# Kernel tuning notes

Measured on AMD Instinct MI355X. Metric: run time of the kernel, lower is better.

## Reference

```python
import math
import jax, jax.numpy as jnp
import numpy as np

B, S, D, H = 64, 577, 768, 12
DH = D // H          # 64 per-head dim
FF = 4 * D           # 3072 intermediate
EPS = 1e-6


def layernorm(x, g, b):
    mu = jnp.mean(x, axis=-1, keepdims=True)
    var = jnp.mean(jnp.square(x - mu), axis=-1, keepdims=True)
    return (x - mu) * jax.lax.rsqrt(var + EPS) * g + b


def gelu_tanh(x):
    # NewGELUActivation: 0.5*x*(1+tanh(sqrt(2/pi)*(x+0.044715*x^3)))
    c = math.sqrt(2.0 / math.pi)
    return 0.5 * x * (1.0 + jnp.tanh(c * (x + 0.044715 * x ** 3)))


def setup_inputs() -> dict:
    key = jax.random.key(0)
    ks = jax.random.split(key, 16)
    s_d = 1.0 / math.sqrt(D)
    s_ff = 1.0 / math.sqrt(FF)
    return {
        "x": jax.random.normal(ks[0], (B, S, D), jnp.float32),
        "ln1_g": jnp.ones((D,), jnp.float32),
        "ln1_b": jnp.zeros((D,), jnp.float32),
        # per-head Q/K/V weights stacked: [H, D, DH] (equivalent to H separate Linears)
        "Wq": jax.random.normal(ks[1], (H, D, DH), jnp.float32) * s_d,
        "bq": jax.random.normal(ks[2], (H, DH), jnp.float32) * 0.01,
        "Wk": jax.random.normal(ks[3], (H, D, DH), jnp.float32) * s_d,
        "bk": jax.random.normal(ks[4], (H, DH), jnp.float32) * 0.01,
        "Wv": jax.random.normal(ks[5], (H, D, DH), jnp.float32) * s_d,
        "bv": jax.random.normal(ks[6], (H, DH), jnp.float32) * 0.01,
        "Wo": jax.random.normal(ks[7], (D, D), jnp.float32) * s_d,
        "bo": jax.random.normal(ks[8], (D,), jnp.float32) * 0.01,
        "ln2_g": jnp.ones((D,), jnp.float32),
        "ln2_b": jnp.zeros((D,), jnp.float32),
        "W1": jax.random.normal(ks[9], (D, FF), jnp.float32) * s_d,
        "b1": jax.random.normal(ks[10], (FF,), jnp.float32) * 0.01,
        "W2": jax.random.normal(ks[11], (FF, D), jnp.float32) * s_ff,
        "b2": jax.random.normal(ks[12], (D,), jnp.float32) * 0.01,
    }


def reference(x, ln1_g, ln1_b, Wq, bq, Wk, bk, Wv, bv, Wo, bo,
              ln2_g, ln2_b, W1, b1, W2, b2):
    # --- pre-norm MHA ---
    h = layernorm(x, ln1_g, ln1_b)                       # [B,S,D]
    q = jnp.einsum('bsd,hde->bhse', h, Wq) + bq[:, None, :]
    k = jnp.einsum('bsd,hde->bhse', h, Wk) + bk[:, None, :]
    v = jnp.einsum('bsd,hde->bhse', h, Wv) + bv[:, None, :]
    scores = jnp.einsum('bhse,bhte->bhst', q, k) / math.sqrt(DH)
    probs = jax.nn.softmax(scores, axis=-1)              # [B,H,S,S]
    attn = jnp.einsum('bhst,bhte->bhse', probs, v)       # [B,H,S,DH]
    # concat heads in head order -> [B,S,H*DH]
    concat = attn.transpose(0, 2, 1, 3).reshape(B, S, H * DH)
    x = x + concat @ Wo + bo
    # --- pre-norm MLP ---
    m = layernorm(x, ln2_g, ln2_b)
    m = gelu_tanh(m @ W1 + b1) @ W2 + b2
    return x + m
```

## Files before the change

kernel.cpp:

```cpp
#include <hip/hip_runtime.h>
#include <stdint.h>

constexpr int BZ   = 64;
constexpr int SEQ  = 577;
constexpr int DM   = 768;
constexpr int NH   = 12;
constexpr int HD   = 64;
constexpr int FFD  = 3072;
constexpr int ROWS = BZ * SEQ;
constexpr int BHN  = BZ * NH;
constexpr int VTS  = 640;

typedef __attribute__((ext_vector_type(8))) short bf16x8;
typedef __attribute__((ext_vector_type(4))) float f32x4;

static __device__ __forceinline__ unsigned short f2bf(float f) {
  union { float f; uint32_t u; } v; v.f = f;
  uint32_t r = (v.u + 0x7FFFu + ((v.u >> 16) & 1u)) >> 16;
  return (unsigned short)r;
}

static __device__ __forceinline__ f32x4 mfma16(bf16x8 a, bf16x8 b, f32x4 c) {
  return __builtin_amdgcn_mfma_f32_16x16x32_bf16(a, b, c, 0, 0, 0);
}

static __device__ __forceinline__ void gload_lds16(const unsigned short* g, unsigned short* l) {
  __builtin_amdgcn_global_load_lds((const __attribute__((address_space(1))) unsigned int*)g,
                                   (__attribute__((address_space(3))) unsigned int*)l, 16, 0, 0);
}

__global__ __launch_bounds__(256) void prep_qkv(const float* __restrict__ Wq,
                                                const float* __restrict__ Wk,
                                                const float* __restrict__ Wv,
                                                unsigned short* __restrict__ dst) {
  int tid = blockIdx.x * 256 + threadIdx.x;
  int n = tid / DM, k = tid - n * DM;
  int seg = n / DM;
  int within = n - seg * DM;
  int h = within >> 6, e = within & 63;
  const float* W = (seg == 0) ? Wq : (seg == 1) ? Wk : Wv;
  dst[tid] = f2bf(W[((size_t)h * DM + k) * HD + e]);
}

__global__ __launch_bounds__(256) void prep_t(const float* __restrict__ src,
                                              unsigned short* __restrict__ dst,
                                              int N, int K) {
  int tid = blockIdx.x * 256 + threadIdx.x;
  if (tid >= N * K) return;
  int n = tid / K, k = tid - n * K;
  dst[tid] = f2bf(src[(size_t)k * N + n]);
}

__global__ __launch_bounds__(256) void ln_bf16(const float* __restrict__ X,
                                               const float* __restrict__ g,
                                               const float* __restrict__ b,
                                               unsigned short* __restrict__ out) {
  int row  = blockIdx.x * 4 + (threadIdx.x >> 6);
  int lane = threadIdx.x & 63;
  const float* x = X + (size_t)row * DM;
  float4 v[3];
  float s = 0.f, s2 = 0.f;
#pragma unroll
  for (int i = 0; i < 3; i++) {
    v[i] = *(const float4*)(x + i * 256 + lane * 4);
    s  += v[i].x + v[i].y + v[i].z + v[i].w;
    s2 += v[i].x * v[i].x + v[i].y * v[i].y + v[i].z * v[i].z + v[i].w * v[i].w;
  }
#pragma unroll
  for (int o = 1; o < 64; o <<= 1) { s += __shfl_xor(s, o); s2 += __shfl_xor(s2, o); }
  float mu  = s * (1.f / DM);
  float var = s2 * (1.f / DM) - mu * mu;
  float inv = rsqrtf(var + 1e-6f);
#pragma unroll
  for (int i = 0; i < 3; i++) {
    int c = i * 256 + lane * 4;
    float4 gg = *(const float4*)(g + c);
    float4 bb = *(const float4*)(b + c);
    ushort4 o4;
    o4.x = f2bf((v[i].x - mu) * inv * gg.x + bb.x);
    o4.y = f2bf((v[i].y - mu) * inv * gg.y + bb.y);
    o4.z = f2bf((v[i].z - mu) * inv * gg.z + bb.z);
    o4.w = f2bf((v[i].w - mu) * inv * gg.w + bb.w);
    *(ushort4*)(out + (size_t)row * DM + c) = o4;
  }
}

template <int EPI>
__global__ __launch_bounds__(512, 2) void gemm_bt(
    const unsigned short* __restrict__ A, const unsigned short* __restrict__ Bt,
    int M, int N, int K, int nbn,
    const float* __restrict__ bias0, const float* __restrict__ bias1,
    const float* __restrict__ bias2, const float* __restrict__ xres,
    float* __restrict__ outf,
    unsigned short* __restrict__ ob0, unsigned short* __restrict__ ob1,
    unsigned short* __restrict__ ob2) {
  __shared__ __align__(16) unsigned short sA[4][256 * 32];
  __shared__ __align__(16) unsigned short sB[4][256 * 32];
  const int tid  = threadIdx.x;
  const int wave = tid >> 6;
  const int lane = tid & 63;
  const int l15 = lane & 15, quad = lane >> 4;
  const int wmi = wave >> 2;
  const int wni = wave & 3;

  const int nb = gridDim.x;
  const int L = blockIdx.x;
  const int per = nb >> 3, rem = nb & 7;
  const int x8 = L & 7, i8 = L >> 3;
  const int g = x8 * per + (x8 < rem ? x8 : rem) + i8;
  const int mt = g / nbn, nt = g - mt * nbn;
  const int m0 = mt * 256, n0 = nt * 256;

  const unsigned short* srcA[2];
  const unsigned short* srcB[2];
  int ldsOff[2];
#pragma unroll
  for (int j = 0; j < 2; j++) {
    int c = tid + j * 512;
    int row = c >> 2, col = c & 3;
    int kc = col ^ (row & 3);
    int ra = m0 + row; if (ra >= M) ra = M - 1;
    srcA[j] = A + (size_t)ra * K + kc * 8;
    srcB[j] = Bt + (size_t)(n0 + row) * K + kc * 8;
    ldsOff[j] = c * 8;
  }

  const int sx8  = (quad ^ (l15 & 3)) * 8;
  const int offAb = (wmi * 128 + l15) * 32 + sx8;
  const int offBb = (wni * 64 + l15) * 32 + sx8;

  f32x4 acc[8][4] = {};
  const int nkt = K >> 5;

#pragma unroll
  for (int tt = 0; tt < 3; ++tt) {
#pragma unroll
    for (int j = 0; j < 2; j++) gload_lds16(srcA[j] + tt * 32, &sA[tt][ldsOff[j]]);
#pragma unroll
    for (int j = 0; j < 2; j++) gload_lds16(srcB[j] + tt * 32, &sB[tt][ldsOff[j]]);
  }
  asm volatile("s_waitcnt vmcnt(8)" ::: "memory");
  __builtin_amdgcn_s_barrier();

  for (int t = 0; t < nkt; ++t) {
    const int rb  = t & 3;
    const int sbf = (t + 3) & 3;
    const bool st = (t + 3) < nkt;
    const size_t koff = (size_t)(t + 3) << 5;
    const unsigned short* sAr = sA[rb];
    const unsigned short* sBr = sB[rb];

    bf16x8 aF[4], bF[4];
#pragma unroll
    for (int mi = 0; mi < 4; mi++) aF[mi] = *(const bf16x8*)(sAr + offAb + mi * 512);
#pragma unroll
    for (int ni = 0; ni < 4; ni++) bF[ni] = *(const bf16x8*)(sBr + offBb + ni * 512);
    if (st) {
      gload_lds16(srcA[0] + koff, &sA[sbf][ldsOff[0]]);
      gload_lds16(srcA[1] + koff, &sA[sbf][ldsOff[1]]);
    }
    __builtin_amdgcn_s_barrier();
    asm volatile("s_waitcnt lgkmcnt(0)" ::: "memory");
    __builtin_amdgcn_sched_barrier(0);
    __builtin_amdgcn_s_setprio(1);
#pragma unroll
    for (int mi = 0; mi < 4; mi++)
#pragma unroll
      for (int ni = 0; ni < 4; ni++) acc[mi][ni] = mfma16(aF[mi], bF[ni], acc[mi][ni]);
    __builtin_amdgcn_s_setprio(0);
    __builtin_amdgcn_s_barrier();

    bf16x8 aG[4];
#pragma unroll
    for (int mi = 0; mi < 4; mi++) aG[mi] = *(const bf16x8*)(sAr + offAb + (mi + 4) * 512);
    if (st) {
      gload_lds16(srcB[0] + koff, &sB[sbf][ldsOff[0]]);
      gload_lds16(srcB[1] + koff, &sB[sbf][ldsOff[1]]);
    }
    __builtin_amdgcn_s_barrier();
    asm volatile("s_waitcnt lgkmcnt(0)" ::: "memory");
    __builtin_amdgcn_sched_barrier(0);
    __builtin_amdgcn_s_setprio(1);
#pragma unroll
    for (int mi = 0; mi < 4; mi++)
#pragma unroll
      for (int ni = 0; ni < 4; ni++) acc[mi + 4][ni] = mfma16(aG[mi], bF[ni], acc[mi + 4][ni]);
    __builtin_amdgcn_s_setprio(0);
    if (st)                   { asm volatile("s_waitcnt vmcnt(8)" ::: "memory"); }
    else if (t + 2 < nkt)     { asm volatile("s_waitcnt vmcnt(4)" ::: "memory"); }
    else if (t + 1 < nkt)     { asm volatile("s_waitcnt vmcnt(0)" ::: "memory"); }
    if (t + 1 < nkt) __builtin_amdgcn_s_barrier();
  }

#pragma unroll
  for (int mi = 0; mi < 8; mi++) {
#pragma unroll
    for (int r = 0; r < 4; r++) {
      int mg = m0 + wmi * 128 + mi * 16 + quad * 4 + r;
      if (mg >= M) continue;
      if constexpr (EPI == 0) {
        int bb = mg / SEQ, ss = mg - bb * SEQ;
        int seg = n0 / DM;
        int within0 = n0 - seg * DM + wni * 64;
#pragma unroll
        for (int ni = 0; ni < 4; ni++) {
          int wcol = within0 + ni * 16 + l15;
          int h = wcol >> 6, e = wcol & 63;
          float val = acc[mi][ni][r];
          if (seg == 0) {
            float qv = (val + bias0[wcol]) * 0.125f;
            ob0[((size_t)(bb * NH + h) * SEQ + ss) * HD + e] = f2bf(qv);
          } else if (seg == 1) {
            float kv = val + bias1[wcol];
            ob1[((size_t)(bb * NH + h) * SEQ + ss) * HD + e] = f2bf(kv);
          } else {
            float vv = val + bias2[wcol];
            ob2[((size_t)(bb * NH + h) * HD + e) * VTS + ss] = f2bf(vv);
          }
        }
      } else if constexpr (EPI == 1) {
        size_t base = (size_t)mg * DM;
#pragma unroll
        for (int ni = 0; ni < 4; ni++) {
          int col = n0 + wni * 64 + ni * 16 + l15;
          outf[base + col] = xres[base + col] + acc[mi][ni][r] + bias0[col];
        }
      } else if constexpr (EPI == 2) {
        size_t base = (size_t)mg * FFD;
#pragma unroll
        for (int ni = 0; ni < 4; ni++) {
          int col = n0 + wni * 64 + ni * 16 + l15;
          float xv = acc[mi][ni][r] + bias0[col];
          float u  = 0.7978845608028654f * (xv + 0.044715f * xv * xv * xv);
          float uc = fminf(fmaxf(u, -15.f), 15.f);
          float t  = __expf(2.f * uc);
          float gel = 0.5f * xv * (1.f + (t - 1.f) / (t + 1.f));
          ob0[base + col] = f2bf(gel);
        }
      } else {
        size_t base = (size_t)mg * DM;
#pragma unroll
        for (int ni = 0; ni < 4; ni++) {
          int col = n0 + wni * 64 + ni * 16 + l15;
          outf[base + col] += acc[mi][ni][r] + bias0[col];
        }
      }
    }
  }
}

__global__ __launch_bounds__(256) void attn_fused(
    const unsigned short* __restrict__ Q, const unsigned short* __restrict__ Kb,
    const unsigned short* __restrict__ Vt, unsigned short* __restrict__ Cc) {
  __shared__ __align__(16) unsigned short sK[64 * 72];
  __shared__ __align__(16) unsigned short sV[64 * 72];
  __shared__ __align__(16) unsigned short sP[4][16 * 72];
  const int tid  = threadIdx.x;
  const int wave = tid >> 6, lane = tid & 63;
  const int quad = lane >> 4, l15 = lane & 15;
  const int bh = blockIdx.y;
  const int q0 = blockIdx.x * 64;

  int qr = q0 + wave * 16 + l15; if (qr > SEQ - 1) qr = SEQ - 1;
  const unsigned short* qrow = Q + ((size_t)bh * SEQ + qr) * HD;
  bf16x8 aQ0 = *(const bf16x8*)(qrow + quad * 8);
  bf16x8 aQ1 = *(const bf16x8*)(qrow + 32 + quad * 8);

  float m[4], l[4];
  f32x4 accO[4] = {};
#pragma unroll
  for (int r = 0; r < 4; r++) { m[r] = -3e38f; l[r] = 0.f; }

  for (int t0 = 0; t0 < SEQ; t0 += 64) {
#pragma unroll
    for (int i = 0; i < 2; i++) {
      int c = tid + i * 256;
      int row = c >> 3, col = (c & 7) << 3;
      int tk = t0 + row; if (tk > SEQ - 1) tk = SEQ - 1;
      bf16x8 vk = *(const bf16x8*)(Kb + ((size_t)bh * SEQ + tk) * HD + col);
      bf16x8 vv = *(const bf16x8*)(Vt + ((size_t)bh * HD + row) * VTS + t0 + col);
      *(bf16x8*)(sK + row * 72 + col) = vk;
      *(bf16x8*)(sV + row * 72 + col) = vv;
    }
    __syncthreads();

    f32x4 s4[4];
#pragma unroll
    for (int ni = 0; ni < 4; ni++) {
      bf16x8 b0 = *(const bf16x8*)(sK + (ni * 16 + l15) * 72 + quad * 8);
      bf16x8 b1 = *(const bf16x8*)(sK + (ni * 16 + l15) * 72 + 32 + quad * 8);
      f32x4 a = {0.f, 0.f, 0.f, 0.f};
      a = mfma16(aQ0, b0, a);
      a = mfma16(aQ1, b1, a);
      s4[ni] = a;
    }
#pragma unroll
    for (int ni = 0; ni < 4; ni++) {
      if (t0 + ni * 16 + l15 >= SEQ) {
#pragma unroll
        for (int r = 0; r < 4; r++) s4[ni][r] = -3e38f;
      }
    }
    float mn[4], alpha[4], ts[4];
#pragma unroll
    for (int r = 0; r < 4; r++) {
      float tm = fmaxf(fmaxf(s4[0][r], s4[1][r]), fmaxf(s4[2][r], s4[3][r]));
#pragma unroll
      for (int o = 1; o < 16; o <<= 1) tm = fmaxf(tm, __shfl_xor(tm, o));
      mn[r] = fmaxf(m[r], tm);
      alpha[r] = __expf(m[r] - mn[r]);
      m[r] = mn[r];
      ts[r] = 0.f;
    }
#pragma unroll
    for (int ni = 0; ni < 4; ni++) {
#pragma unroll
      for (int r = 0; r < 4; r++) {
        float p = __expf(s4[ni][r] - mn[r]);
        ts[r] += p;
        sP[wave][(quad * 4 + r) * 72 + ni * 16 + l15] = f2bf(p);
      }
    }
#pragma unroll
    for (int r = 0; r < 4; r++) {
#pragma unroll
      for (int o = 1; o < 16; o <<= 1) ts[r] += __shfl_xor(ts[r], o);
      l[r] = l[r] * alpha[r] + ts[r];
#pragma unroll
      for (int ni = 0; ni < 4; ni++) accO[ni][r] *= alpha[r];
    }
    bf16x8 aP0 = *(const bf16x8*)(sP[wave] + l15 * 72 + quad * 8);
    bf16x8 aP1 = *(const bf16x8*)(sP[wave] + l15 * 72 + 32 + quad * 8);
#pragma unroll
    for (int ni = 0; ni < 4; ni++) {
      bf16x8 v0 = *(const bf16x8*)(sV + (ni * 16 + l15) * 72 + quad * 8);
      bf16x8 v1 = *(const bf16x8*)(sV + (ni * 16 + l15) * 72 + 32 + quad * 8);
      accO[ni] = mfma16(aP0, v0, accO[ni]);
      accO[ni] = mfma16(aP1, v1, accO[ni]);
    }
    __syncthreads();
  }

  int bb = bh / NH, h = bh - bb * NH;
#pragma unroll
  for (int r = 0; r < 4; r++) {
    int ss = q0 + wave * 16 + quad * 4 + r;
    if (ss < SEQ) {
      float inv = 1.f / l[r];
      size_t base = ((size_t)bb * SEQ + ss) * DM + h * HD;
#pragma unroll
      for (int ni = 0; ni < 4; ni++)
        Cc[base + ni * 16 + l15] = f2bf(accO[ni][r] * inv);
    }
  }
}

extern "C" void kernel_launch(void* const* d_in, const int* in_sizes, int n_in,
                              void* d_out, int out_size, void* d_ws, size_t ws_size,
                              hipStream_t stream) {
  (void)in_sizes; (void)n_in; (void)out_size; (void)ws_size;
  const float* x     = (const float*)d_in[0];
  const float* ln1_g = (const float*)d_in[1];
  const float* ln1_b = (const float*)d_in[2];
  const float* Wq    = (const float*)d_in[3];
  const float* bq    = (const float*)d_in[4];
  const float* Wk    = (const float*)d_in[5];
  const float* bk    = (const float*)d_in[6];
  const float* Wv    = (const float*)d_in[7];
  const float* bv    = (const float*)d_in[8];
  const float* Wo    = (const float*)d_in[9];
  const float* bo    = (const float*)d_in[10];
  const float* ln2_g = (const float*)d_in[11];
  const float* ln2_b = (const float*)d_in[12];
  const float* W1    = (const float*)d_in[13];
  const float* b1    = (const float*)d_in[14];
  const float* W2    = (const float*)d_in[15];
  const float* b2    = (const float*)d_in[16];
  float* out = (float*)d_out;

  char* ws = (char*)d_ws;
  size_t off = 0;
  auto alloc = [&](size_t bytes) -> unsigned short* {
    unsigned short* p = (unsigned short*)(ws + off);
    off += (bytes + 255) & ~(size_t)255;
    return p;
  };
  unsigned short* h_bf  = alloc((size_t)ROWS * DM * 2);
  unsigned short* q_bf  = alloc((size_t)BHN * SEQ * HD * 2);
  unsigned short* k_bf  = alloc((size_t)BHN * SEQ * HD * 2);
  unsigned short* vt_bf = alloc((size_t)BHN * HD * VTS * 2);
  unsigned short* cc_bf = alloc((size_t)ROWS * DM * 2);
  unsigned short* g_bf = q_bf;
  unsigned short* wqkv_t = alloc((size_t)2304 * 768 * 2);
  unsigned short* w1_t   = alloc((size_t)3072 * 768 * 2);
  unsigned short* w2_t   = alloc((size_t)768 * 3072 * 2);
  unsigned short* wo_t   = alloc((size_t)768 * 768 * 2);

  prep_qkv<<<(2304 * 768) / 256, 256, 0, stream>>>(Wq, Wk, Wv, wqkv_t);
  prep_t<<<(3072 * 768) / 256, 256, 0, stream>>>(W1, w1_t, 3072, 768);
  prep_t<<<(768 * 3072) / 256, 256, 0, stream>>>(W2, w2_t, 768, 3072);
  prep_t<<<(768 * 768) / 256, 256, 0, stream>>>(Wo, wo_t, 768, 768);

  const int MB2 = (ROWS + 255) / 256;

  ln_bf16<<<ROWS / 4, 256, 0, stream>>>(x, ln1_g, ln1_b, h_bf);
  gemm_bt<0><<<MB2 * 9, 512, 0, stream>>>(
      h_bf, wqkv_t, ROWS, 2304, 768, 9, bq, bk, bv, nullptr, nullptr, q_bf, k_bf, vt_bf);
  attn_fused<<<dim3((SEQ + 63) / 64, BHN), 256, 0, stream>>>(q_bf, k_bf, vt_bf, cc_bf);
  gemm_bt<1><<<MB2 * 3, 512, 0, stream>>>(
      cc_bf, wo_t, ROWS, 768, 768, 3, bo, nullptr, nullptr, x, out, nullptr, nullptr, nullptr);
  ln_bf16<<<ROWS / 4, 256, 0, stream>>>(out, ln2_g, ln2_b, h_bf);
  gemm_bt<2><<<MB2 * 12, 512, 0, stream>>>(
      h_bf, w1_t, ROWS, 3072, 768, 12, b1, nullptr, nullptr, nullptr, nullptr, g_bf, nullptr, nullptr);
  gemm_bt<3><<<MB2 * 3, 512, 0, stream>>>(
      g_bf, w2_t, ROWS, 768, 3072, 3, b2, nullptr, nullptr, nullptr, out, nullptr, nullptr, nullptr);
}
```

Before: 1.570 ms.

## Switch GEMM to BK=64 double-buffered LDS pipeline with 8-way swizzle

Restructures the bf16 GEMM main loop from a 4-stage BK=32 ring buffer into a 2-stage BK=64 double buffer. Each iteration issues all next-tile loads at once and runs four MFMA sub-phases over two K halves, using an XOR swizzle widened to 8 columns. The goal is fewer loop iterations and less barrier and wait overhead per K element. The cost is shallower prefetch depth: only one tile is in flight, and a full vmcnt(0) wait each iteration may expose memory latency.

Measured after the change: 1.691 ms. +7.7%, slower.

```diff
diff --git a/kernel.cpp b/kernel.cpp
--- a/kernel.cpp
+++ b/kernel.cpp
@@ -94,8 +94,8 @@
     float* __restrict__ outf,
     unsigned short* __restrict__ ob0, unsigned short* __restrict__ ob1,
     unsigned short* __restrict__ ob2) {
-  __shared__ __align__(16) unsigned short sA[4][256 * 32];
-  __shared__ __align__(16) unsigned short sB[4][256 * 32];
+  __shared__ __align__(16) unsigned short sA[2][256 * 64];
+  __shared__ __align__(16) unsigned short sB[2][256 * 64];
   const int tid  = threadIdx.x;
   const int wave = tid >> 6;
   const int lane = tid & 63;
@@ -111,53 +111,54 @@
   const int mt = g / nbn, nt = g - mt * nbn;
   const int m0 = mt * 256, n0 = nt * 256;
 
-  const unsigned short* srcA[2];
-  const unsigned short* srcB[2];
-  int ldsOff[2];
-#pragma unroll
-  for (int j = 0; j < 2; j++) {
+  const unsigned short* srcA[4];
+  const unsigned short* srcB[4];
+  int ldsOff[4];
+#pragma unroll
+  for (int j = 0; j < 4; j++) {
     int c = tid + j * 512;
-    int row = c >> 2, col = c & 3;
-    int kc = col ^ (row & 3);
+    int row = c >> 3, col = c & 7;
+    int kc = col ^ (row & 7);
     int ra = m0 + row; if (ra >= M) ra = M - 1;
     srcA[j] = A + (size_t)ra * K + kc * 8;
     srcB[j] = Bt + (size_t)(n0 + row) * K + kc * 8;
     ldsOff[j] = c * 8;
   }
 
-  const int sx8  = (quad ^ (l15 & 3)) * 8;
-  const int offAb = (wmi * 128 + l15) * 32 + sx8;
-  const int offBb = (wni * 64 + l15) * 32 + sx8;
+  const int sw0 = ((0 << 2) | quad) ^ (l15 & 7);
+  const int sw1 = ((1 << 2) | quad) ^ (l15 & 7);
+  const int arow = (wmi * 128 + l15) * 64;
+  const int brow = (wni * 64 + l15) * 64;
 
   f32x4 acc[8][4] = {};
-  const int nkt = K >> 5;
-
-#pragma unroll
-  for (int tt = 0; tt < 3; ++tt) {
-#pragma unroll
-    for (int j = 0; j < 2; j++) gload_lds16(srcA[j] + tt * 32, &sA[tt][ldsOff[j]]);
-#pragma unroll
-    for (int j = 0; j < 2; j++) gload_lds16(srcB[j] + tt * 32, &sB[tt][ldsOff[j]]);
-  }
-  asm volatile("s_waitcnt vmcnt(8)" ::: "memory");
+  const int nkt = K >> 6;
+
+#pragma unroll
+  for (int j = 0; j < 4; j++) gload_lds16(srcA[j], &sA[0][ldsOff[j]]);
+#pragma unroll
+  for (int j = 0; j < 4; j++) gload_lds16(srcB[j], &sB[0][ldsOff[j]]);
+  asm volatile("s_waitcnt vmcnt(0)" ::: "memory");
   __builtin_amdgcn_s_barrier();
 
   for (int t = 0; t < nkt; ++t) {
-    const int rb  = t & 3;
-    const int sbf = (t + 3) & 3;
-    const bool st = (t + 3) < nkt;
-    const size_t koff = (size_t)(t + 3) << 5;
-    const unsigned short* sAr = sA[rb];
-    const unsigned short* sBr = sB[rb];
-
-    bf16x8 aF[4], bF[4];
-#pragma unroll
-    for (int mi = 0; mi < 4; mi++) aF[mi] = *(const bf16x8*)(sAr + offAb + mi * 512);
-#pragma unroll
-    for (int ni = 0; ni < 4; ni++) bF[ni] = *(const bf16x8*)(sBr + offBb + ni * 512);
+    const int p = t & 1;
+    const bool st = (t + 1) < nkt;
+    const size_t koff = (size_t)(t + 1) << 6;
+    const unsigned short* pa = sA[p];
+    const unsigned short* pb = sB[p];
+    unsigned short* na = sA[p ^ 1];
+    unsigned short* nb_ = sB[p ^ 1];
+
+    bf16x8 aF[4], bF[4], aG[4];
+#pragma unroll
+    for (int mi = 0; mi < 4; mi++) aF[mi] = *(const bf16x8*)(pa + arow + mi * 1024 + sw0 * 8);
+#pragma unroll
+    for (int ni = 0; ni < 4; ni++) bF[ni] = *(const bf16x8*)(pb + brow + ni * 1024 + sw0 * 8);
     if (st) {
-      gload_lds16(srcA[0] + koff, &sA[sbf][ldsOff[0]]);
-      gload_lds16(srcA[1] + koff, &sA[sbf][ldsOff[1]]);
+#pragma unroll
+      for (int j = 0; j < 4; j++) gload_lds16(srcA[j] + koff, &na[ldsOff[j]]);
+#pragma unroll
+      for (int j = 0; j < 4; j++) gload_lds16(srcB[j] + koff, &nb_[ldsOff[j]]);
     }
     __builtin_amdgcn_s_barrier();
     asm volatile("s_waitcnt lgkmcnt(0)" ::: "memory");
@@ -170,13 +171,8 @@
     __builtin_amdgcn_s_setprio(0);
     __builtin_amdgcn_s_barrier();
 
-    bf16x8 aG[4];
-#pragma unroll
-    for (int mi = 0; mi < 4; mi++) aG[mi] = *(const bf16x8*)(sAr + offAb + (mi + 4) * 512);
-    if (st) {
-      gload_lds16(srcB[0] + koff, &sB[sbf][ldsOff[0]]);
-      gload_lds16(srcB[1] + koff, &sB[sbf][ldsOff[1]]);
-    }
+#pragma unroll
+    for (int mi = 0; mi < 4; mi++) aG[mi] = *(const bf16x8*)(pa + arow + (mi + 4) * 1024 + sw0 * 8);
     __builtin_amdgcn_s_barrier();
     asm volatile("s_waitcnt lgkmcnt(0)" ::: "memory");
     __builtin_amdgcn_sched_barrier(0);
@@ -186,10 +182,38 @@
 #pragma unroll
       for (int ni = 0; ni < 4; ni++) acc[mi + 4][ni] = mfma16(aG[mi], bF[ni], acc[mi + 4][ni]);
     __builtin_amdgcn_s_setprio(0);
-    if (st)                   { asm volatile("s_waitcnt vmcnt(8)" ::: "memory"); }
-    else if (t + 2 < nkt)     { asm volatile("s_waitcnt vmcnt(4)" ::: "memory"); }
-    else if (t + 1 < nkt)     { asm volatile("s_waitcnt vmcnt(0)" ::: "memory"); }
-    if (t + 1 < nkt) __builtin_amdgcn_s_barrier();
+    __builtin_amdgcn_s_barrier();
+
+#pragma unroll
+    for (int mi = 0; mi < 4; mi++) aF[mi] = *(const bf16x8*)(pa + arow + mi * 1024 + sw1 * 8);
+#pragma unroll
+    for (int ni = 0; ni < 4; ni++) bF[ni] = *(const bf16x8*)(pb + brow + ni * 1024 + sw1 * 8);
+    __builtin_amdgcn_s_barrier();
+    asm volatile("s_waitcnt lgkmcnt(0)" ::: "memory");
+    __builtin_amdgcn_sched_barrier(0);
+    __builtin_amdgcn_s_setprio(1);
+#pragma unroll
+    for (int mi = 0; mi < 4; mi++)
+#pragma unroll
+      for (int ni = 0; ni < 4; ni++) acc[mi][ni] = mfma16(aF[mi], bF[ni], acc[mi][ni]);
+    __builtin_amdgcn_s_setprio(0);
+    __builtin_amdgcn_s_barrier();
+
+#pragma unroll
+    for (int mi = 0; mi < 4; mi++) aG[mi] = *(const bf16x8*)(pa + arow + (mi + 4) * 1024 + sw1 * 8);
+    __builtin_amdgcn_s_barrier();
+    asm volatile("s_waitcnt lgkmcnt(0)" ::: "memory");
+    __builtin_amdgcn_sched_barrier(0);
+    __builtin_amdgcn_s_setprio(1);
+#pragma unroll
+    for (int mi = 0; mi < 4; mi++)
+#pragma unroll
+      for (int ni = 0; ni < 4; ni++) acc[mi + 4][ni] = mfma16(aG[mi], bF[ni], acc[mi + 4][ni]);
+    __builtin_amdgcn_s_setprio(0);
+    if (st) {
+      asm volatile("s_waitcnt vmcnt(0)" ::: "memory");
+      __builtin_amdgcn_s_barrier();
+    }
   }
 
 #pragma unroll
```
